# Kernel tuning notes

Measured on AMD Instinct MI355X. Metric: run time of the kernel, lower is better.

## Reference

```python
import jax, jax.numpy as jnp
import numpy as np

B, S, D, H, OUT = 64, 512, 128, 2, 8
TD, VD, AD = 300, 35, 74
DH = D // H
EPS = 1e-5


def _layernorm(x, g, b):
    m = jnp.mean(x, -1, keepdims=True)
    v = jnp.var(x, -1, keepdims=True)
    return (x - m) * jax.lax.rsqrt(v + EPS) * g + b


def _attn_neg(q_in, k_in, v_in, Wq, bq, Wk, bk, Wv, bv, Wd, bd, g, beta):
    # MultiheadAttention2: probs = 1 - softmax(scores). dropout off (eval).
    b_, s_, _ = q_in.shape
    q = (q_in @ Wq + bq).reshape(b_, s_, H, DH).transpose(0, 2, 1, 3)
    k = (k_in @ Wk + bk).reshape(b_, k_in.shape[1], H, DH).transpose(0, 2, 1, 3)
    v = (v_in @ Wv + bv).reshape(b_, v_in.shape[1], H, DH).transpose(0, 2, 1, 3)
    scores = jnp.einsum('bhqd,bhkd->bhqk', q, k) / jnp.sqrt(jnp.float32(DH))
    probs = 1.0 - jax.nn.softmax(scores, axis=-1)
    ctx = jnp.einsum('bhqk,bhkd->bhqd', probs, v)
    ctx = ctx.transpose(0, 2, 1, 3).reshape(b_, s_, D)
    return _layernorm(ctx @ Wd + bd, g, beta)


def _gru_dir(x, Wih, Whh, bih, bhh):
    # torch GRU, gate order (r, z, n). x: [B,S,D] -> [B,S,H=128]
    gx = x @ Wih.T + bih  # [B,S,3H]
    gx_t = gx.transpose(1, 0, 2)  # [S,B,3H]

    def step(h, g_t):
        gh = h @ Whh.T + bhh
        xr, xz, xn = jnp.split(g_t, 3, -1)
        hr, hz, hn = jnp.split(gh, 3, -1)
        r = jax.nn.sigmoid(xr + hr)
        z = jax.nn.sigmoid(xz + hz)
        n = jnp.tanh(xn + r * hn)
        h_new = (1.0 - z) * n + z * h
        return h_new, h_new

    h0 = jnp.zeros((x.shape[0], D), x.dtype)
    _, hs = jax.lax.scan(step, h0, gx_t)
    return hs.transpose(1, 0, 2)


def _bigru(x, Wih, Whh, bih, bhh):
    fwd = _gru_dir(x, Wih[0], Whh[0], bih[0], bhh[0])
    bwd = _gru_dir(x[:, ::-1], Wih[1], Whh[1], bih[1], bhh[1])[:, ::-1]
    return jnp.concatenate([fwd, bwd], -1)


def setup_inputs() -> dict:
    key = jax.random.key(0)
    ks = iter(jax.random.split(key, 40))
    sc = 0.05

    def rn(shape, s=sc):
        return jax.random.normal(next(ks), shape, jnp.float32) * s

    inp = {
        'text_features': rn((B, S, TD), 1.0),
        'visual_features': rn((B, S, VD), 1.0),
        'audio_features': rn((B, S, AD), 1.0),
        'fc1W': rn((TD, D)), 'fc1b': rn((D,)),
        'fc2W': rn((VD, D)), 'fc2b': rn((D,)),
        'fc3W': rn((AD, D)), 'fc3b': rn((D,)),
        # 6 attention units: [ta_a, ta_b, tv_a, tv_b, va_a, va_b]
        'Wq': rn((6, D, D)), 'bq': rn((6, D)),
        'Wk': rn((6, D, D)), 'bk': rn((6, D)),
        'Wv': rn((6, D, D)), 'bv': rn((6, D)),
        'Wd': rn((6, D, D)), 'bd': rn((6, D)),
        'ln_g': jnp.ones((6, D), jnp.float32), 'ln_b': jnp.zeros((6, D), jnp.float32),
        # 3 bidirectional GRUs: [gru1(text), gru2(visual), gru3(audio)] x [fwd, bwd]
        'gWih': rn((3, 2, 3 * D, D)), 'gWhh': rn((3, 2, 3 * D, D)),
        'gbih': rn((3, 2, 3 * D)), 'gbhh': rn((3, 2, 3 * D)),
        # head: Linear(3D,2D) -> BN(eval) -> ReLU6 -> Linear(2D,out)
        'fW1': rn((3 * D, 2 * D)), 'fb1': rn((2 * D,)),
        'bn_g': jnp.ones((2 * D,), jnp.float32), 'bn_b': jnp.zeros((2 * D,), jnp.float32),
        'fW2': rn((2 * D, OUT)), 'fb2': rn((OUT,)),
    }
    return inp


def reference(text_features, visual_features, audio_features,
              fc1W, fc1b, fc2W, fc2b, fc3W, fc3b,
              Wq, bq, Wk, bk, Wv, bv, Wd, bd, ln_g, ln_b,
              gWih, gWhh, gbih, gbhh,
              fW1, fb1, bn_g, bn_b, fW2, fb2):
    t = text_features @ fc1W + fc1b
    v = visual_features @ fc2W + fc2b
    a = audio_features @ fc3W + fc3b

    def A(i, q, k, val):
        return _attn_neg(q, k, val, Wq[i], bq[i], Wk[i], bk[i], Wv[i], bv[i],
                         Wd[i], bd[i], ln_g[i], ln_b[i])

    # CrossAttention(a,b): b_out = a_attn(a,b,b); a_out = b_attn(b,a,a)
    audio_out1 = A(0, t, a, a)   # text_audio.a_attention
    text_out1 = A(1, a, t, t)    # text_audio.b_attention
    visual_out1 = A(2, t, v, v)  # text_visual.a_attention
    text_out2 = A(3, v, t, t)    # text_visual.b_attention
    audio_out2 = A(4, v, a, a)   # visual_audio.a_attention
    visual_out2 = A(5, a, v, v)  # visual_audio.b_attention

    text_out = (text_out1 + text_out2) / 2
    visual_out = (visual_out1 + visual_out2) / 2
    audio_out = (audio_out1 + audio_out2) / 2

    text_out = _bigru(text_out, gWih[0], gWhh[0], gbih[0], gbhh[0])
    visual_out = _bigru(visual_out, gWih[1], gWhh[1], gbih[1], gbhh[1])
    audio_out = _bigru(audio_out, gWih[2], gWhh[2], gbih[2], gbhh[2])

    out = jnp.concatenate([text_out, visual_out, audio_out], -1)  # [B,S,6D]
    out = jnp.mean((out[:, :, 3 * D:] + out[:, :, :3 * D]) / 2, axis=1)  # [B,3D]

    h = out @ fW1 + fb1
    # BatchNorm1d in eval with running stats (mean=0, var=1)
    h = h * jax.lax.rsqrt(jnp.float32(1.0 + EPS)) * bn_g + bn_b
    h = jnp.clip(h, 0.0, 6.0)  # ReLU6
    return h @ fW2 + fb2
```

## Files before the change

### kernel.cpp

```cpp
#include <hip/hip_runtime.h>
#include <hip/hip_bf16.h>

#define BB 64
#define SS 512
#define DD 128
#define NROW (BB * SS)
#define SZ ((size_t)NROW * DD)

#define LOG2E 1.4426950408889634f
#define QSCALE (0.125f * LOG2E)

typedef __attribute__((ext_vector_type(8))) short short8;
typedef __attribute__((ext_vector_type(4))) float f32x4;

#define WB_P1 0
#define WB_P2 40960
#define WB_P3 49152
#define WB_QKVD 61440
#define WB_WIH 454656
#define WB_WHH 749568
#define WB_TOTAL 1044480

__device__ __forceinline__ float frcp_(float x) { return __builtin_amdgcn_rcpf(x); }
__device__ __forceinline__ float fexp2_(float x) { return __builtin_amdgcn_exp2f(x); }
__device__ __forceinline__ float b2f(unsigned short u) {
  union { unsigned int i; float f; } x; x.i = ((unsigned int)u) << 16; return x.f;
}
__device__ __forceinline__ unsigned short f2b(float f) {
  __hip_bfloat16 b = __float2bfloat16(f);
  return *reinterpret_cast<unsigned short*>(&b);
}
__device__ __forceinline__ unsigned short f2b_trunc(float f) {
  union { float f; unsigned int i; } x; x.f = f; return (unsigned short)(x.i >> 16);
}

__global__ __launch_bounds__(256) void prep_kernel(
    const float* __restrict__ fc1W, const float* __restrict__ fc2W,
    const float* __restrict__ fc3W, const float* __restrict__ Wq,
    const float* __restrict__ Wk, const float* __restrict__ Wv,
    const float* __restrict__ Wd, const float* __restrict__ gWih,
    const float* __restrict__ gWhh, const float* __restrict__ gbih,
    const float* __restrict__ gbhh, const float* __restrict__ bq,
    unsigned short* __restrict__ WB, float* __restrict__ gbihs,
    float* __restrict__ bqs) {
  for (int idx = blockIdx.x * 256 + threadIdx.x; idx < WB_TOTAL;
       idx += gridDim.x * 256) {
    float v;
    if (idx < WB_P2) {
      int n = idx / 320, k = idx % 320;
      v = (k < 300) ? fc1W[k * 128 + n] : 0.f;
    } else if (idx < WB_P3) {
      int r = idx - WB_P2; int n = r >> 6, k = r & 63;
      v = (k < 35) ? fc2W[k * 128 + n] : 0.f;
    } else if (idx < WB_QKVD) {
      int r = idx - WB_P3; int n = r / 96, k = r % 96;
      v = (k < 74) ? fc3W[k * 128 + n] : 0.f;
    } else if (idx < WB_WIH) {
      int r = idx - WB_QKVD;
      int op = r / 98304; int r2 = r % 98304;
      int u = r2 >> 14; int r3 = r2 & 16383;
      int n = r3 >> 7, k = r3 & 127;
      const float* src = (op == 0) ? Wq : (op == 1) ? Wk : (op == 2) ? Wv : Wd;
      v = src[u * 16384 + k * 128 + n];
      if (op == 0) v *= QSCALE;
    } else if (idx < WB_WHH) {
      int r = idx - WB_WIH;
      int r3 = r % 49152;
      int gate = (r3 >> 7) >> 7;
      v = gWih[r] * (gate < 2 ? LOG2E : 2.f * LOG2E);
    } else {
      int r = idx - WB_WHH;
      int r3 = r % 49152;
      int gate = (r3 >> 7) >> 7;
      v = gWhh[r] * (gate < 2 ? LOG2E : 2.f * LOG2E);
    }
    WB[idx] = f2b(v);
  }
  for (int idx = blockIdx.x * 256 + threadIdx.x; idx < 6 * 384;
       idx += gridDim.x * 256) {
    int gate = (idx % 384) >> 7;
    float v = gbih[idx] + (gate < 2 ? gbhh[idx] : 0.f);
    gbihs[idx] = v * (gate < 2 ? LOG2E : 2.f * LOG2E);
  }
  for (int idx = blockIdx.x * 256 + threadIdx.x; idx < 6 * 128;
       idx += gridDim.x * 256) {
    bqs[idx] = bq[idx] * QSCALE;
  }
}

struct GArg {
  const void* A; const unsigned short* W; const float* bias; void* C;
  int Ka, Kp, abf, cbf, cs; float* vsum;
};
struct GArgs { GArg g[18]; };

__global__ __launch_bounds__(256) void gemm_b(GArgs args) {
  const GArg ga = args.g[blockIdx.z];
  const int ny = blockIdx.y;
  __shared__ unsigned short As[128 * 40];
  __shared__ unsigned short Ws[128 * 40];
  const int t = threadIdx.x;
  const int w = t >> 6, lane = t & 63, q = lane >> 4, lm = lane & 15;
  const int wm = w >> 1, wn = w & 1;
  const int m0 = blockIdx.x * 128;
  const int row = t >> 1, cb = (t & 1) * 16;
  f32x4 acc[4][4];
#pragma unroll
  for (int i = 0; i < 4; ++i)
#pragma unroll
    for (int j = 0; j < 4; ++j) acc[i][j] = (f32x4){0.f, 0.f, 0.f, 0.f};

  for (int kt = 0; kt < ga.Kp; kt += 32) {
    if (ga.abf) {
      const unsigned short* Ag =
          (const unsigned short*)ga.A + (size_t)(m0 + row) * ga.Ka + kt + cb;
      short8 v0 = *reinterpret_cast<const short8*>(Ag);
      short8 v1 = *reinterpret_cast<const short8*>(Ag + 8);
      *reinterpret_cast<short8*>(&As[row * 40 + cb]) = v0;
      *reinterpret_cast<short8*>(&As[row * 40 + cb + 8]) = v1;
    } else {
      const float* Ag = (const float*)ga.A + (size_t)(m0 + row) * ga.Ka + kt + cb;
      unsigned short tmp[16];
#pragma unroll
      for (int j = 0; j < 16; ++j) {
        int k = kt + cb + j;
        tmp[j] = (k < ga.Ka) ? f2b(Ag[j]) : 0;
      }
      *reinterpret_cast<short8*>(&As[row * 40 + cb]) =
          *reinterpret_cast<short8*>(&tmp[0]);
      *reinterpret_cast<short8*>(&As[row * 40 + cb + 8]) =
          *reinterpret_cast<short8*>(&tmp[8]);
    }
    {
      const unsigned short* Wg =
          ga.W + (size_t)(ny * 128 + row) * ga.Kp + kt + cb;
      short8 v0 = *reinterpret_cast<const short8*>(Wg);
      short8 v1 = *reinterpret_cast<const short8*>(Wg + 8);
      *reinterpret_cast<short8*>(&Ws[row * 40 + cb]) = v0;
      *reinterpret_cast<short8*>(&Ws[row * 40 + cb + 8]) = v1;
    }
    __syncthreads();
    short8 af[4], bfv[4];
#pragma unroll
    for (int mi = 0; mi < 4; ++mi)
      af[mi] = *reinterpret_cast<const short8*>(
          &As[(wm * 64 + mi * 16 + lm) * 40 + q * 8]);
#pragma unroll
    for (int ni = 0; ni < 4; ++ni)
      bfv[ni] = *reinterpret_cast<const short8*>(
          &Ws[(wn * 64 + ni * 16 + lm) * 40 + q * 8]);
#pragma unroll
    for (int mi = 0; mi < 4; ++mi)
#pragma unroll
      for (int ni = 0; ni < 4; ++ni)
        acc[mi][ni] = __builtin_amdgcn_mfma_f32_16x16x32_bf16(
            af[mi], bfv[ni], acc[mi][ni], 0, 0, 0);
    __syncthreads();
  }
#pragma unroll
  for (int ni = 0; ni < 4; ++ni) {
    const int colg = ny * 128 + wn * 64 + ni * 16 + lm;
    const float bv = ga.bias[colg];
#pragma unroll
    for (int mi = 0; mi < 4; ++mi) {
      const int rg = m0 + wm * 64 + mi * 16 + q * 4;
#pragma unroll
      for (int r = 0; r < 4; ++r) {
        float v = acc[mi][ni][r] + bv;
        if (ga.cbf)
          ((unsigned short*)ga.C)[(size_t)(rg + r) * ga.cs + colg] = f2b(v);
        else
          ((float*)ga.C)[(size_t)(rg + r) * ga.cs + colg] = v;
      }
    }
  }
  if (ga.vsum) {
    float* vp = ga.vsum + (size_t)(m0 >> 9) * 128;
#pragma unroll
    for (int ni = 0; ni < 4; ++ni) {
      const int colg = wn * 64 + ni * 16 + lm;
      float s = 16.f * ga.bias[colg];
#pragma unroll
      for (int mi = 0; mi < 4; ++mi)
#pragma unroll
        for (int r = 0; r < 4; ++r) s += acc[mi][ni][r];
      atomicAdd(&vp[colg], s);
    }
  }
}

__global__ __launch_bounds__(256) void attn2(
    const unsigned short* __restrict__ QKV, const float* __restrict__ VS,
    unsigned short* __restrict__ CTX) {
  __shared__ unsigned short Vt[64 * 72];
  __shared__ unsigned short Pt[4][16 * 72];
  const int t = threadIdx.x;
  const int w = t >> 6, lane = t & 63, quad = lane >> 4, lm = lane & 15;
  const int z = blockIdx.z;
  const int bh = blockIdx.y, b = bh >> 1, h = bh & 1;
  const int qbase = blockIdx.x * 256;

  const unsigned short* Qg = QKV + (size_t)(z * 3 + 0) * SZ;
  const unsigned short* Kg = QKV + (size_t)(z * 3 + 1) * SZ;
  const unsigned short* Vg = QKV + (size_t)(z * 3 + 2) * SZ;

  short8 aq[4][2];
#pragma unroll
  for (int qt = 0; qt < 4; ++qt)
#pragma unroll
    for (int c = 0; c < 2; ++c)
      aq[qt][c] = *reinterpret_cast<const short8*>(
          Qg + ((size_t)(b * SS + qbase + qt * 64 + w * 16 + lm)) * DD +
          h * 64 + c * 32 + quad * 8);

  const f32x4 czero = {0.f, 0.f, 0.f, 0.f};
  f32x4 o[4][4];
#pragma unroll
  for (int i = 0; i < 4; ++i)
#pragma unroll
    for (int j = 0; j < 4; ++j) o[i][j] = czero;
  float suml[4][4];
#pragma unroll
  for (int i = 0; i < 4; ++i)
#pragma unroll
    for (int j = 0; j < 4; ++j) suml[i][j] = 0.f;

  const int vk = t >> 3, vd0 = (t & 7) * 8;

  for (int kt = 0; kt < 8; ++kt) {
    const int k0 = kt * 64;
    __syncthreads();
#pragma unroll
    for (int i = 0; i < 2; ++i) {
      const int k = vk + i * 32;
      short8 vv = *reinterpret_cast<const short8*>(
          Vg + ((size_t)(b * SS + k0 + k)) * DD + h * 64 + vd0);
#pragma unroll
      for (int j = 0; j < 8; ++j) {
        const int d = vd0 + j;
        Vt[d * 72 + (k ^ (d & 56))] = (unsigned short)vv[j];
      }
    }
    __syncthreads();

    short8 bk[4][2];
#pragma unroll
    for (int nt = 0; nt < 4; ++nt)
#pragma unroll
      for (int c = 0; c < 2; ++c)
        bk[nt][c] = *reinterpret_cast<const short8*>(
            Kg + ((size_t)(b * SS + k0 + nt * 16 + lm)) * DD + h * 64 +
            c * 32 + quad * 8);
    short8 bvv[4][2];
#pragma unroll
    for (int dt = 0; dt < 4; ++dt) {
      const int d = dt * 16 + lm;
#pragma unroll
      for (int c = 0; c < 2; ++c)
        bvv[dt][c] = *reinterpret_cast<const short8*>(
            &Vt[d * 72 + ((c * 32 + quad * 8) ^ (d & 56))]);
    }

#pragma unroll
    for (int qt = 0; qt < 4; ++qt) {
      f32x4 sacc[4];
#pragma unroll
      for (int nt = 0; nt < 4; ++nt)
        sacc[nt] = __builtin_amdgcn_mfma_f32_16x16x32_bf16(
            aq[qt][0], bk[nt][0], czero, 0, 0, 0);
#pragma unroll
      for (int nt = 0; nt < 4; ++nt)
        sacc[nt] = __builtin_amdgcn_mfma_f32_16x16x32_bf16(
            aq[qt][1], bk[nt][1], sacc[nt], 0, 0, 0);
#pragma unroll
      for (int nt = 0; nt < 4; ++nt) {
#pragma unroll
        for (int r = 0; r < 4; ++r) {
          float p = fexp2_(sacc[nt][r]);
          suml[qt][r] += p;
          Pt[w][(quad * 4 + r) * 72 + nt * 16 + lm] = f2b_trunc(p);
        }
      }
#pragma unroll
      for (int c = 0; c < 2; ++c) {
        short8 ap = *reinterpret_cast<const short8*>(
            &Pt[w][lm * 72 + c * 32 + quad * 8]);
#pragma unroll
        for (int dt = 0; dt < 4; ++dt)
          o[qt][dt] = __builtin_amdgcn_mfma_f32_16x16x32_bf16(
              ap, bvv[dt][c], o[qt][dt], 0, 0, 0);
      }
    }
  }
#pragma unroll
  for (int qt = 0; qt < 4; ++qt)
#pragma unroll
    for (int r = 0; r < 4; ++r) {
#pragma unroll
      for (int m = 1; m < 16; m <<= 1)
        suml[qt][r] += __shfl_xor(suml[qt][r], m);
    }
  const float* vsp = VS + (size_t)(z * BB + b) * DD + h * 64;
#pragma unroll
  for (int qt = 0; qt < 4; ++qt)
#pragma unroll
    for (int dt = 0; dt < 4; ++dt) {
      const int col = dt * 16 + lm;
      const float vs = vsp[col];
#pragma unroll
      for (int r = 0; r < 4; ++r) {
        const int row = qbase + qt * 64 + w * 16 + quad * 4 + r;
        CTX[(size_t)z * SZ + ((size_t)(b * SS + row)) * DD + h * 64 + col] =
            f2b(vs - o[qt][dt][r] * frcp_(suml[qt][r]));
      }
    }
}

__global__ __launch_bounds__(256) void ln_pair(
    const unsigned short* __restrict__ DOUT, const float* __restrict__ lng,
    const float* __restrict__ lnb, unsigned short* __restrict__ GRUIN) {
  const int g = blockIdx.y;
  const int row = blockIdx.x * 4 + (threadIdx.x >> 6);
  const int t = threadIdx.x & 63;
  const int u1t[3] = {1, 2, 0};
  const int u2t[3] = {3, 5, 4};
  float outA = 0.f, outB = 0.f;
#pragma unroll
  for (int half = 0; half < 2; ++half) {
    const int u = half == 0 ? u1t[g] : u2t[g];
    const unsigned short* x = DOUT + (size_t)u * SZ + (size_t)row * DD;
    float a = b2f(x[t]), c = b2f(x[t + 64]);
    float s = a + c, sq = a * a + c * c;
#pragma unroll
    for (int off = 32; off > 0; off >>= 1) {
      s += __shfl_down(s, off);
      sq += __shfl_down(sq, off);
    }
    s = __shfl(s, 0); sq = __shfl(sq, 0);
    float mean = s * (1.f / 128.f);
    float var = sq * (1.f / 128.f) - mean * mean;
    float rs = rsqrtf(var + 1e-5f);
    const float* gg = lng + u * 128;
    const float* bb = lnb + u * 128;
    outA += (a - mean) * rs * gg[t] + bb[t];
    outB += (c - mean) * rs * gg[t + 64] + bb[t + 64];
  }
  unsigned short* op = GRUIN + (size_t)g * SZ + (size_t)row * DD;
  op[t] = f2b(0.5f * outA);
  op[t + 64] = f2b(0.5f * outB);
}

#define AST 136

__global__ __launch_bounds__(512, 1) void gru8(
    const unsigned short* __restrict__ GXR, const unsigned short* __restrict__ WB,
    const float* __restrict__ gbhh, float* __restrict__ HS) {
  __shared__ unsigned short Abuf[2][16 * AST];
  const int rec = blockIdx.y, bg = blockIdx.x;
  const int dir = rec & 1;
  const int t = threadIdx.x;
  const int w = t >> 6, lane = t & 63, q = lane >> 4, lm = lane & 15;
  const int o = w * 16 + lm;
  const int b = bg * 4 + q;

  short8 Bh[3][4];
  const unsigned short* whh = WB + WB_WHH + (size_t)rec * 49152;
#pragma unroll
  for (int gate = 0; gate < 3; ++gate)
#pragma unroll
    for (int c = 0; c < 4; ++c)
      Bh[gate][c] = *reinterpret_cast<const short8*>(
          whh + (size_t)(gate * 128 + o) * 128 + c * 32 + q * 8);
  const float bhn = gbhh[rec * 384 + 256 + o] * (2.f * LOG2E);
  const f32x4 czero = {0.f, 0.f, 0.f, 0.f};
  const f32x4 cbhn = {bhn, 0.f, 0.f, 0.f};

  float h = 0.f, hsum = 0.f;
  for (int i = t; i < 2 * 16 * AST; i += 512)
    (&Abuf[0][0])[i] = 0;

  const unsigned short* gx0 = GXR + (size_t)rec * 12582912 +
      ((size_t)b * 512 + (dir ? 511 : 0)) * 384 + o;
  const ptrdiff_t st = dir ? -384 : 384;

  unsigned short ring[4][3];
#pragma unroll
  for (int pp = 0; pp < 4; ++pp) {
    const unsigned short* gp = gx0 + (ptrdiff_t)pp * st;
#pragma unroll
    for (int j = 0; j < 3; ++j) ring[pp][j] = gp[j * 128];
  }
  const unsigned short* pf = gx0 + (ptrdiff_t)4 * st;
  __syncthreads();

#pragma unroll 4
  for (int s = 0; s < SS; ++s) {
    const int p = s & 1, slot = s & 3;
    const float gxr = b2f(ring[slot][0]);
    const float gxz = b2f(ring[slot][1]);
    const float gxn = b2f(ring[slot][2]);
#pragma unroll
    for (int j = 0; j < 3; ++j) ring[slot][j] = pf[j * 128];
    pf += (s < SS - 5) ? st : 0;

    short8 ah0 = *reinterpret_cast<const short8*>(&Abuf[p][lm * AST + 0 + q * 8]);
    short8 ah1 = *reinterpret_cast<const short8*>(&Abuf[p][lm * AST + 32 + q * 8]);
    short8 ah2 = *reinterpret_cast<const short8*>(&Abuf[p][lm * AST + 64 + q * 8]);
    short8 ah3 = *reinterpret_cast<const short8*>(&Abuf[p][lm * AST + 96 + q * 8]);
    f32x4 r0 = __builtin_amdgcn_mfma_f32_16x16x32_bf16(ah0, Bh[0][0], czero, 0, 0, 0);
    f32x4 r1 = __builtin_amdgcn_mfma_f32_16x16x32_bf16(ah2, Bh[0][2], czero, 0, 0, 0);
    f32x4 z0 = __builtin_amdgcn_mfma_f32_16x16x32_bf16(ah0, Bh[1][0], czero, 0, 0, 0);
    f32x4 z1 = __builtin_amdgcn_mfma_f32_16x16x32_bf16(ah2, Bh[1][2], czero, 0, 0, 0);
    f32x4 n0 = __builtin_amdgcn_mfma_f32_16x16x32_bf16(ah0, Bh[2][0], cbhn, 0, 0, 0);
    f32x4 n1 = __builtin_amdgcn_mfma_f32_16x16x32_bf16(ah2, Bh[2][2], czero, 0, 0, 0);
    r0 = __builtin_amdgcn_mfma_f32_16x16x32_bf16(ah1, Bh[0][1], r0, 0, 0, 0);
    r1 = __builtin_amdgcn_mfma_f32_16x16x32_bf16(ah3, Bh[0][3], r1, 0, 0, 0);
    z0 = __builtin_amdgcn_mfma_f32_16x16x32_bf16(ah1, Bh[1][1], z0, 0, 0, 0);
    z1 = __builtin_amdgcn_mfma_f32_16x16x32_bf16(ah3, Bh[1][3], z1, 0, 0, 0);
    n0 = __builtin_amdgcn_mfma_f32_16x16x32_bf16(ah1, Bh[2][1], n0, 0, 0, 0);
    n1 = __builtin_amdgcn_mfma_f32_16x16x32_bf16(ah3, Bh[2][3], n1, 0, 0, 0);

    float rr = frcp_(1.f + fexp2_(-(gxr + r0[0] + r1[0])));
    float zz = frcp_(1.f + fexp2_(-(gxz + z0[0] + z1[0])));
    float nn = 1.f - 2.f * frcp_(fexp2_(gxn + rr * (n0[0] + n1[0])) + 1.f);
    h = nn + zz * (h - nn);
    hsum += h;
    Abuf[p ^ 1][(q * 4) * AST + o] = f2b_trunc(h);
    asm volatile("s_waitcnt lgkmcnt(0)\n\ts_barrier" ::: "memory");
  }
  HS[((size_t)rec * BB + bg * 4 + q) * 128 + o] = hsum;
}

__global__ __launch_bounds__(256) void head_kernel(
    const float* __restrict__ HS, const float* __restrict__ fW1,
    const float* __restrict__ fb1, const float* __restrict__ bng,
    const float* __restrict__ bnb, const float* __restrict__ fW2,
    const float* __restrict__ fb2, float* __restrict__ out) {
  __shared__ float pl[384];
  __shared__ float h1[256];
  int b = blockIdx.x, n = threadIdx.x;
  {
    int j = n;
    int seg = j >> 7, oo = j & 127;
    pl[j] = (HS[((size_t)seg * BB + b) * 128 + oo] +
             HS[((size_t)(seg + 3) * BB + b) * 128 + oo]) * (0.5f / 512.f);
  }
  if (n < 128) {
    int j = 256 + n;
    int seg = j >> 7, oo = j & 127;
    pl[j] = (HS[((size_t)seg * BB + b) * 128 + oo] +
             HS[((size_t)(seg + 3) * BB + b) * 128 + oo]) * (0.5f / 512.f);
  }
  __syncthreads();
  float acc = fb1[n];
  for (int k = 0; k < 384; ++k) acc += pl[k] * fW1[k * 256 + n];
  float hv = acc * rsqrtf(1.f + 1e-5f) * bng[n] + bnb[n];
  hv = fminf(fmaxf(hv, 0.f), 6.f);
  h1[n] = hv;
  __syncthreads();
  if (n < 8) {
    float a2 = fb2[n];
    for (int k = 0; k < 256; ++k) a2 += h1[k] * fW2[k * 8 + n];
    out[b * 8 + n] = a2;
  }
}

extern "C" void kernel_launch(void* const* d_in, const int* in_sizes, int n_in,
                              void* d_out, int out_size, void* d_ws,
                              size_t ws_size, hipStream_t stream) {
  (void)in_sizes; (void)n_in; (void)out_size; (void)ws_size;
  const float* text = (const float*)d_in[0];
  const float* vis  = (const float*)d_in[1];
  const float* aud  = (const float*)d_in[2];
  const float* fc1W = (const float*)d_in[3];
  const float* fc1b = (const float*)d_in[4];
  const float* fc2W = (const float*)d_in[5];
  const float* fc2b = (const float*)d_in[6];
  const float* fc3W = (const float*)d_in[7];
  const float* fc3b = (const float*)d_in[8];
  const float* Wq = (const float*)d_in[9];
  const float* bq = (const float*)d_in[10];
  const float* Wk = (const float*)d_in[11];
  const float* bk = (const float*)d_in[12];
  const float* Wv = (const float*)d_in[13];
  const float* bv = (const float*)d_in[14];
  const float* Wd = (const float*)d_in[15];
  const float* bd = (const float*)d_in[16];
  const float* lng = (const float*)d_in[17];
  const float* lnb = (const float*)d_in[18];
  const float* gWih = (const float*)d_in[19];
  const float* gWhh = (const float*)d_in[20];
  const float* gbih = (const float*)d_in[21];
  const float* gbhh = (const float*)d_in[22];
  const float* fW1 = (const float*)d_in[23];
  const float* fb1 = (const float*)d_in[24];
  const float* bng = (const float*)d_in[25];
  const float* bnb = (const float*)d_in[26];
  const float* fW2 = (const float*)d_in[27];
  const float* fb2 = (const float*)d_in[28];
  float* out = (float*)d_out;

  unsigned short* WSB = (unsigned short*)d_ws;
  unsigned short* T   = WSB;
  unsigned short* Vv  = WSB + SZ;
  unsigned short* Aa  = WSB + 2 * SZ;
  unsigned short* QKV = WSB + 3 * SZ;
  unsigned short* CTX = WSB + 12 * SZ;
  unsigned short* DOUT = WSB;
  unsigned short* GXR = WSB;
  unsigned short* GRUIN = WSB + 18 * SZ;
  unsigned short* WB  = WSB + 21 * SZ;
  float* VS = (float*)(WSB + 21 * SZ + 1048576);
  float* HS = VS + 6 * 64 * 128;
  float* gbihs = HS + 6 * 64 * 128;
  float* bqs = gbihs + 6 * 384;

  prep_kernel<<<dim3(1024), dim3(256), 0, stream>>>(
      fc1W, fc2W, fc3W, Wq, Wk, Wv, Wd, gWih, gWhh, gbih, gbhh, bq, WB,
      gbihs, bqs);
  hipMemsetAsync(VS, 0, 6 * 64 * 128 * sizeof(float), stream);

  {
    GArgs ga{};
    ga.g[0] = {text, WB + WB_P1, fc1b, T, 300, 320, 0, 1, 128};
    ga.g[1] = {vis,  WB + WB_P2, fc2b, Vv, 35, 64, 0, 1, 128};
    ga.g[2] = {aud,  WB + WB_P3, fc3b, Aa, 74, 96, 0, 1, 128};
    gemm_b<<<dim3(256, 1, 3), dim3(256), 0, stream>>>(ga);
  }

  const int qsel[6] = {0, 2, 0, 1, 1, 2};
  const int ksel[6] = {2, 0, 1, 0, 2, 1};
  unsigned short* proj[3] = {T, Vv, Aa};

  for (int phase = 0; phase < 2; ++phase) {
    GArgs ga{};
    for (int ul = 0; ul < 3; ++ul) {
      int u = phase * 3 + ul;
      for (int op = 0; op < 3; ++op) {
        int z = ul * 3 + op;
        const float* bias = (op == 0) ? (bqs + u * 128)
                          : (op == 1) ? (bk + u * 128) : (bv + u * 128);
        float* vsum = (op == 2) ? (VS + (size_t)(phase * 3 + ul) * BB * DD)
                                : nullptr;
        ga.g[z] = {proj[op == 0 ? qsel[u] : ksel[u]],
                   WB + WB_QKVD + op * 98304 + u * 16384, bias,
                   QKV + (size_t)z * SZ, 128, 128, 1, 1, 128, vsum};
      }
    }
    gemm_b<<<dim3(256, 1, 9), dim3(256), 0, stream>>>(ga);
    attn2<<<dim3(2, 128, 3), dim3(256), 0, stream>>>(
        QKV, VS + phase * 3 * BB * DD, CTX + (size_t)phase * 3 * SZ);
  }

  {
    GArgs ga{};
    for (int u = 0; u < 6; ++u)
      ga.g[u] = {CTX + (size_t)u * SZ, WB + WB_QKVD + 3 * 98304 + u * 16384,
                 bd + u * 128, DOUT + (size_t)u * SZ, 128, 128, 1, 1, 128};
    gemm_b<<<dim3(256, 1, 6), dim3(256), 0, stream>>>(ga);
  }

  ln_pair<<<dim3(NROW / 4, 3), dim3(256), 0, stream>>>(DOUT, lng, lnb, GRUIN);

  {
    GArgs ga{};
    for (int r6 = 0; r6 < 6; ++r6) {
      int g = r6 >> 1;
      ga.g[r6] = {GRUIN + (size_t)g * SZ, WB + WB_WIH + r6 * 49152,
                  gbihs + r6 * 384, GXR + (size_t)r6 * 12582912,
                  128, 128, 1, 1, 384};
    }
    gemm_b<<<dim3(256, 3, 6), dim3(256), 0, stream>>>(ga);
  }

  gru8<<<dim3(16, 6), dim3(512), 0, stream>>>(GXR, WB, gbhh, HS);
  head_kernel<<<dim3(BB), dim3(256), 0, stream>>>(HS, fW1, fb1, bng, bnb, fW2, fb2, out);
}
```

Before: 763.9 us.

## Shorten GRU step critical path with independent MFMA chains and swizzled LDS

The GRU recurrence kernel now issues twelve independent MFMAs instead of two dependent chains. The input-gate terms for r and z are folded into the MFMA accumulator initialisation, and the update is rewritten with fma to shorten the serial dependency per timestep. The hidden-state LDS buffer shrinks to 4 rows with an XOR swizzle so the write and the four reads avoid bank conflicts. The layernorm-pair kernel switches to packed 32-bit loads and stores of bf16 pairs. The extra MFMA results must be summed by scalar adds, which adds some VALU work per step.

```diff
diff --git a/kernel.cpp b/kernel.cpp
--- a/kernel.cpp
+++ b/kernel.cpp
@@ -329,7 +329,9 @@
   for (int half = 0; half < 2; ++half) {
     const int u = half == 0 ? u1t[g] : u2t[g];
     const unsigned short* x = DOUT + (size_t)u * SZ + (size_t)row * DD;
-    float a = b2f(x[t]), c = b2f(x[t + 64]);
+    unsigned int xv = *reinterpret_cast<const unsigned int*>(x + 2 * t);
+    float a = b2f((unsigned short)(xv & 0xffffu));
+    float c = b2f((unsigned short)(xv >> 16));
     float s = a + c, sq = a * a + c * c;
 #pragma unroll
     for (int off = 32; off > 0; off >>= 1) {
@@ -342,12 +344,13 @@
     float rs = rsqrtf(var + 1e-5f);
     const float* gg = lng + u * 128;
     const float* bb = lnb + u * 128;
-    outA += (a - mean) * rs * gg[t] + bb[t];
-    outB += (c - mean) * rs * gg[t + 64] + bb[t + 64];
+    outA += (a - mean) * rs * gg[2 * t] + bb[2 * t];
+    outB += (c - mean) * rs * gg[2 * t + 1] + bb[2 * t + 1];
   }
   unsigned short* op = GRUIN + (size_t)g * SZ + (size_t)row * DD;
-  op[t] = f2b(0.5f * outA);
-  op[t + 64] = f2b(0.5f * outB);
+  unsigned int pk = (unsigned int)f2b(0.5f * outA) |
+                    ((unsigned int)f2b(0.5f * outB) << 16);
+  *reinterpret_cast<unsigned int*>(op + 2 * t) = pk;
 }
 
 #define AST 136
@@ -355,13 +358,14 @@
 __global__ __launch_bounds__(512, 1) void gru8(
     const unsigned short* __restrict__ GXR, const unsigned short* __restrict__ WB,
     const float* __restrict__ gbhh, float* __restrict__ HS) {
-  __shared__ unsigned short Abuf[2][16 * AST];
+  __shared__ unsigned short Abuf[2][4 * AST];
   const int rec = blockIdx.y, bg = blockIdx.x;
   const int dir = rec & 1;
   const int t = threadIdx.x;
   const int w = t >> 6, lane = t & 63, q = lane >> 4, lm = lane & 15;
   const int o = w * 16 + lm;
   const int b = bg * 4 + q;
+  const int a4 = lm >> 2;
 
   short8 Bh[3][4];
   const unsigned short* whh = WB + WB_WHH + (size_t)rec * 49152;
@@ -373,11 +377,13 @@
           whh + (size_t)(gate * 128 + o) * 128 + c * 32 + q * 8);
   const float bhn = gbhh[rec * 384 + 256 + o] * (2.f * LOG2E);
   const f32x4 czero = {0.f, 0.f, 0.f, 0.f};
-  const f32x4 cbhn = {bhn, 0.f, 0.f, 0.f};
 
   float h = 0.f, hsum = 0.f;
-  for (int i = t; i < 2 * 16 * AST; i += 512)
+  for (int i = t; i < 2 * 4 * AST; i += 512)
     (&Abuf[0][0])[i] = 0;
+
+  const int rb = a4 * AST + q * 8;
+  const int wro = q * AST + ((((o >> 5) ^ q) & 3) << 5) + (o & 31);
 
   const unsigned short* gx0 = GXR + (size_t)rec * 12582912 +
       ((size_t)b * 512 + (dir ? 511 : 0)) * 384 + o;
@@ -403,29 +409,41 @@
     for (int j = 0; j < 3; ++j) ring[slot][j] = pf[j * 128];
     pf += (s < SS - 5) ? st : 0;
 
-    short8 ah0 = *reinterpret_cast<const short8*>(&Abuf[p][lm * AST + 0 + q * 8]);
-    short8 ah1 = *reinterpret_cast<const short8*>(&Abuf[p][lm * AST + 32 + q * 8]);
-    short8 ah2 = *reinterpret_cast<const short8*>(&Abuf[p][lm * AST + 64 + q * 8]);
-    short8 ah3 = *reinterpret_cast<const short8*>(&Abuf[p][lm * AST + 96 + q * 8]);
-    f32x4 r0 = __builtin_amdgcn_mfma_f32_16x16x32_bf16(ah0, Bh[0][0], czero, 0, 0, 0);
-    f32x4 r1 = __builtin_amdgcn_mfma_f32_16x16x32_bf16(ah2, Bh[0][2], czero, 0, 0, 0);
-    f32x4 z0 = __builtin_amdgcn_mfma_f32_16x16x32_bf16(ah0, Bh[1][0], czero, 0, 0, 0);
-    f32x4 z1 = __builtin_amdgcn_mfma_f32_16x16x32_bf16(ah2, Bh[1][2], czero, 0, 0, 0);
-    f32x4 n0 = __builtin_amdgcn_mfma_f32_16x16x32_bf16(ah0, Bh[2][0], cbhn, 0, 0, 0);
-    f32x4 n1 = __builtin_amdgcn_mfma_f32_16x16x32_bf16(ah2, Bh[2][2], czero, 0, 0, 0);
-    r0 = __builtin_amdgcn_mfma_f32_16x16x32_bf16(ah1, Bh[0][1], r0, 0, 0, 0);
-    r1 = __builtin_amdgcn_mfma_f32_16x16x32_bf16(ah3, Bh[0][3], r1, 0, 0, 0);
-    z0 = __builtin_amdgcn_mfma_f32_16x16x32_bf16(ah1, Bh[1][1], z0, 0, 0, 0);
-    z1 = __builtin_amdgcn_mfma_f32_16x16x32_bf16(ah3, Bh[1][3], z1, 0, 0, 0);
-    n0 = __builtin_amdgcn_mfma_f32_16x16x32_bf16(ah1, Bh[2][1], n0, 0, 0, 0);
-    n1 = __builtin_amdgcn_mfma_f32_16x16x32_bf16(ah3, Bh[2][3], n1, 0, 0, 0);
-
-    float rr = frcp_(1.f + fexp2_(-(gxr + r0[0] + r1[0])));
-    float zz = frcp_(1.f + fexp2_(-(gxz + z0[0] + z1[0])));
-    float nn = 1.f - 2.f * frcp_(fexp2_(gxn + rr * (n0[0] + n1[0])) + 1.f);
-    h = nn + zz * (h - nn);
+    f32x4 cgr = czero; cgr[0] = gxr;
+    f32x4 cgz = czero; cgz[0] = gxz;
+    f32x4 cbn = czero; cbn[0] = bhn;
+
+    short8 ah0 = *reinterpret_cast<const short8*>(&Abuf[p][rb + ((0 ^ a4) << 5)]);
+    short8 ah1 = *reinterpret_cast<const short8*>(&Abuf[p][rb + ((1 ^ a4) << 5)]);
+    short8 ah2 = *reinterpret_cast<const short8*>(&Abuf[p][rb + ((2 ^ a4) << 5)]);
+    short8 ah3 = *reinterpret_cast<const short8*>(&Abuf[p][rb + ((3 ^ a4) << 5)]);
+
+    f32x4 r0 = __builtin_amdgcn_mfma_f32_16x16x32_bf16(ah0, Bh[0][0], cgr, 0, 0, 0);
+    f32x4 r1 = __builtin_amdgcn_mfma_f32_16x16x32_bf16(ah1, Bh[0][1], czero, 0, 0, 0);
+    f32x4 r2 = __builtin_amdgcn_mfma_f32_16x16x32_bf16(ah2, Bh[0][2], czero, 0, 0, 0);
+    f32x4 r3 = __builtin_amdgcn_mfma_f32_16x16x32_bf16(ah3, Bh[0][3], czero, 0, 0, 0);
+    f32x4 z0 = __builtin_amdgcn_mfma_f32_16x16x32_bf16(ah0, Bh[1][0], cgz, 0, 0, 0);
+    f32x4 z1 = __builtin_amdgcn_mfma_f32_16x16x32_bf16(ah1, Bh[1][1], czero, 0, 0, 0);
+    f32x4 z2 = __builtin_amdgcn_mfma_f32_16x16x32_bf16(ah2, Bh[1][2], czero, 0, 0, 0);
+    f32x4 z3 = __builtin_amdgcn_mfma_f32_16x16x32_bf16(ah3, Bh[1][3], czero, 0, 0, 0);
+    f32x4 n0 = __builtin_amdgcn_mfma_f32_16x16x32_bf16(ah0, Bh[2][0], cbn, 0, 0, 0);
+    f32x4 n1 = __builtin_amdgcn_mfma_f32_16x16x32_bf16(ah1, Bh[2][1], czero, 0, 0, 0);
+    f32x4 n2 = __builtin_amdgcn_mfma_f32_16x16x32_bf16(ah2, Bh[2][2], czero, 0, 0, 0);
+    f32x4 n3 = __builtin_amdgcn_mfma_f32_16x16x32_bf16(ah3, Bh[2][3], czero, 0, 0, 0);
+
+    float rs = (r0[0] + r1[0]) + (r2[0] + r3[0]);
+    float zs = (z0[0] + z1[0]) + (z2[0] + z3[0]);
+    float ns = (n0[0] + n1[0]) + (n2[0] + n3[0]);
+
+    float rr = frcp_(1.f + fexp2_(-rs));
+    float zz = frcp_(1.f + fexp2_(-zs));
+    float omz = 1.f - zz;
+    float t1 = fmaf(zz, h, omz);
+    float t2 = -2.f * omz;
+    float ww = frcp_(fexp2_(gxn + rr * ns) + 1.f);
+    h = fmaf(t2, ww, t1);
     hsum += h;
-    Abuf[p ^ 1][(q * 4) * AST + o] = f2b_trunc(h);
+    Abuf[p ^ 1][wro] = f2b_trunc(h);
     asm volatile("s_waitcnt lgkmcnt(0)\n\ts_barrier" ::: "memory");
   }
   HS[((size_t)rec * BB + bg * 4 + q) * 128 + o] = hsum;
```

Result: slower. 793.3 us (+3.9%).
